# Optimization experiments

Hardware: AMD Instinct MI355X
Metric: run time of the kernel (lower is better)

## Reference

```python
import jax, jax.numpy as jnp
import numpy as np

DIM = 256
NUM_HEADS = 8
HEAD_DIM = DIM // NUM_HEADS
SCALE = HEAD_DIM ** -0.5


def setup_inputs() -> dict:
    key = jax.random.key(0)
    ks = jax.random.split(key, 12)
    B, NQ, S = 2, 1024, 8192
    inp = {
        "query_vectors": jax.random.normal(ks[0], (B, NQ, DIM), jnp.float32),
        "key_input_flatten": jax.random.normal(ks[1], (B, S, DIM), jnp.float32),
        "value_input_flatten": jax.random.normal(ks[2], (B, S, DIM), jnp.float32),
        "attention_mask": jax.random.randint(ks[3], (B, S), 0, 2).astype(jnp.float32),
        # Linear params (torch convention: y = x @ W.T + b)
        "Wq": jax.random.normal(ks[4], (DIM, DIM), jnp.float32) / np.sqrt(DIM),
        "bq": jnp.zeros((DIM,), jnp.float32),
        "Wk": jax.random.normal(ks[5], (DIM, DIM), jnp.float32) / np.sqrt(DIM),
        "bk": jnp.zeros((DIM,), jnp.float32),
        "Wv": jax.random.normal(ks[6], (DIM, DIM), jnp.float32) / np.sqrt(DIM),
        "bv": jnp.zeros((DIM,), jnp.float32),
        "Wo": jax.random.normal(ks[7], (DIM, DIM), jnp.float32) / np.sqrt(DIM),
        "bo": jnp.zeros((DIM,), jnp.float32),
    }
    return inp


def _split_heads(x):
    # (B, N, D) -> (B, H, N, hd)
    B, N, D = x.shape
    return x.reshape(B, N, NUM_HEADS, HEAD_DIM).transpose(0, 2, 1, 3)


def reference(query_vectors, key_input_flatten, value_input_flatten, attention_mask,
              Wq, bq, Wk, bk, Wv, bv, Wo, bo):
    B, NQ, D = query_vectors.shape
    q = _split_heads(query_vectors @ Wq.T + bq) * SCALE          # (B,H,NQ,hd)
    k = _split_heads(key_input_flatten @ Wk.T + bk)              # (B,H,S,hd)
    v = _split_heads(value_input_flatten @ Wv.T + bv)            # (B,H,S,hd)
    scores = jnp.einsum('bhqd,bhkd->bhqk', q, k)                 # (B,H,NQ,S)
    scores = scores + attention_mask[:, None, None, :] * -100.0
    finfo = jnp.finfo(scores.dtype)
    scores = jnp.clip(scores, finfo.min, finfo.max)
    probs = jax.nn.softmax(scores, axis=-1)
    ctx = jnp.einsum('bhqk,bhkd->bhqd', probs, v)                # (B,H,NQ,hd)
    ctx = ctx.transpose(0, 2, 1, 3).reshape(B, NQ, D)
    return ctx @ Wo.T + bo
```

## Files before the change

### kernel.cpp

```cpp
#include <hip/hip_runtime.h>
#include <hip/hip_bf16.h>

typedef __bf16 bf16x8 __attribute__((ext_vector_type(8)));
typedef __bf16 bf16x4 __attribute__((ext_vector_type(4)));
typedef float  f32x4  __attribute__((ext_vector_type(4)));

constexpr int BATCH = 2, H = 8, NQ = 1024, SEQ = 8192, DIM = 256, HD = 32;
constexpr int CHUNKS = 8, KVCHUNK = SEQ / CHUNKS;
constexpr float SCALE = 0.17677669529663687f;
constexpr float LOG2E = 1.4426950408889634f;
constexpr float QSCALE = SCALE * LOG2E;
constexpr float MASKC = 100.0f * LOG2E;
constexpr float MFIX  = 12.0f;

constexpr size_t OFF_QH   = 0;
constexpr size_t OFF_KH   = OFF_QH  + (size_t)BATCH*H*NQ*HD*2;
constexpr size_t OFF_VT   = OFF_KH  + (size_t)BATCH*H*SEQ*HD*2;
constexpr size_t OFF_CTX  = OFF_VT  + (size_t)BATCH*H*SEQ*HD*2;
constexpr size_t OFF_W    = OFF_CTX + (size_t)BATCH*NQ*DIM*4;
constexpr size_t OFF_PL   = OFF_W   + (size_t)4*DIM*DIM*2;
constexpr size_t OFF_BIAS = OFF_PL  + (size_t)CHUNKS*16*NQ*4;
constexpr size_t OFF_PO   = OFF_BIAS + (size_t)BATCH*SEQ*4;

__device__ __forceinline__ float fast_exp2(float x) {
    return __builtin_amdgcn_exp2f(x);
}

__global__ void prep_weights_kernel(const float* __restrict__ Wq, const float* __restrict__ Wk,
                                    const float* __restrict__ Wv, const float* __restrict__ Wo,
                                    const float* __restrict__ mask,
                                    __bf16* __restrict__ out, float* __restrict__ biasv) {
    int i = blockIdx.x * 256 + threadIdx.x;
    out[i]          = (__bf16)(Wq[i] * QSCALE);
    out[65536 + i]  = (__bf16)(Wk[i]);
    out[131072 + i] = (__bf16)(Wv[i]);
    out[196608 + i] = (__bf16)(Wo[i]);
    if (i < BATCH * SEQ)
        biasv[i] = -(mask[i] * MASKC + MFIX);
}

__global__ __launch_bounds__(256, 2)
void qkv_proj_kernel(const float* __restrict__ Xq, const float* __restrict__ Xk,
                     const float* __restrict__ Xv, const __bf16* __restrict__ Wb,
                     const float* __restrict__ bq, const float* __restrict__ bk,
                     const float* __restrict__ bv,
                     __bf16* __restrict__ qh, __bf16* __restrict__ kh, __bf16* __restrict__ vtp)
{
    __shared__ __bf16 Ash[128][72];
    __shared__ __bf16 Bsh[128][72];
    const int bid = blockIdx.x;
    const float* X; const __bf16* W; const float* bias; float bscale;
    __bf16* outp; int Mb, mode, lbid;
    if (bid < 32)       { X = Xq; W = Wb;          bias = bq; bscale = QSCALE; outp = qh;  Mb = NQ;  mode = 0; lbid = bid; }
    else if (bid < 288) { X = Xk; W = Wb + 65536;  bias = bk; bscale = 1.f;    outp = kh;  Mb = SEQ; mode = 0; lbid = bid - 32; }
    else                { X = Xv; W = Wb + 131072; bias = bv; bscale = 1.f;    outp = vtp; Mb = SEQ; mode = 1; lbid = bid - 288; }

    const int m0 = (lbid >> 1) * 128;
    const int n0 = (lbid & 1) * 128;
    const int t = threadIdx.x;
    const int w = t >> 6;
    const int lane = t & 63;
    const int g = lane >> 4;
    const int lr = lane & 15;
    const int wr = w >> 1, wc = w & 1;

    f32x4 acc[4][4] = {};

    for (int kk = 0; kk < DIM; kk += 64) {
        __syncthreads();
        #pragma unroll
        for (int i = 0; i < 8; ++i) {
            int c = i * 256 + t;
            int row = c >> 4;
            int q = c & 15;
            const float4 v = *reinterpret_cast<const float4*>(X + (size_t)(m0 + row) * DIM + kk + q * 4);
            bf16x4 bvv;
            bvv[0] = (__bf16)v.x; bvv[1] = (__bf16)v.y; bvv[2] = (__bf16)v.z; bvv[3] = (__bf16)v.w;
            *reinterpret_cast<bf16x4*>(&Ash[row][q * 4]) = bvv;
        }
        #pragma unroll
        for (int i = 0; i < 4; ++i) {
            int c = i * 256 + t;
            int row = c >> 3;
            int q = c & 7;
            *reinterpret_cast<bf16x8*>(&Bsh[row][q * 8]) =
                *reinterpret_cast<const bf16x8*>(W + (size_t)(n0 + row) * DIM + kk + q * 8);
        }
        __syncthreads();

        #pragma unroll
        for (int ks = 0; ks < 2; ++ks) {
            bf16x8 af[4], bfr[4];
            #pragma unroll
            for (int mt = 0; mt < 4; ++mt)
                af[mt] = *reinterpret_cast<const bf16x8*>(&Ash[wr * 64 + mt * 16 + lr][ks * 32 + g * 8]);
            #pragma unroll
            for (int nt = 0; nt < 4; ++nt)
                bfr[nt] = *reinterpret_cast<const bf16x8*>(&Bsh[wc * 64 + nt * 16 + lr][ks * 32 + g * 8]);
            if (mode == 1) {
                #pragma unroll
                for (int mt = 0; mt < 4; ++mt)
                    #pragma unroll
                    for (int nt = 0; nt < 4; ++nt)
                        acc[mt][nt] = __builtin_amdgcn_mfma_f32_16x16x32_bf16(bfr[nt], af[mt], acc[mt][nt], 0, 0, 0);
            } else {
                #pragma unroll
                for (int mt = 0; mt < 4; ++mt)
                    #pragma unroll
                    for (int nt = 0; nt < 4; ++nt)
                        acc[mt][nt] = __builtin_amdgcn_mfma_f32_16x16x32_bf16(af[mt], bfr[nt], acc[mt][nt], 0, 0, 0);
            }
        }
    }

    const int bb = m0 / Mb;
    const int sbase = m0 - bb * Mb + wr * 64;

    if (mode == 0) {
        #pragma unroll
        for (int nt = 0; nt < 4; ++nt) {
            int n = n0 + wc * 64 + nt * 16 + lr;
            float bvv = bias[n] * bscale;
            int h = n >> 5, hd = n & 31;
            __bf16* op = outp + ((size_t)(bb * H + h) * Mb) * 32 + hd;
            #pragma unroll
            for (int mt = 0; mt < 4; ++mt)
                #pragma unroll
                for (int r = 0; r < 4; ++r) {
                    int s = sbase + mt * 16 + g * 4 + r;
                    op[(size_t)s * 32] = (__bf16)(acc[mt][nt][r] + bvv);
                }
        }
    } else {
        #pragma unroll
        for (int nt = 0; nt < 4; ++nt)
            #pragma unroll
            for (int r = 0; r < 4; ++r) {
                int n = n0 + wc * 64 + nt * 16 + g * 4 + r;
                float bvv = bias[n] * bscale;
                int h = n >> 5, hd = n & 31;
                __bf16* op = outp + ((size_t)(bb * H + h) * 32 + hd) * SEQ;
                #pragma unroll
                for (int mt = 0; mt < 4; ++mt) {
                    int s = sbase + mt * 16 + lr;
                    op[s] = (__bf16)(acc[mt][nt][r] + bvv);
                }
            }
    }
}

__global__ __launch_bounds__(256, 2)
void oproj_kernel(const float* __restrict__ X, const __bf16* __restrict__ W,
                  const float* __restrict__ bias, float* __restrict__ outf)
{
    __shared__ __bf16 Ash[128][72];
    __shared__ __bf16 Bsh[128][72];
    const int m0 = (blockIdx.x >> 1) * 128;
    const int n0 = (blockIdx.x & 1) * 128;
    const int t = threadIdx.x;
    const int w = t >> 6;
    const int lane = t & 63;
    const int g = lane >> 4;
    const int lr = lane & 15;
    const int wr = w >> 1, wc = w & 1;

    f32x4 acc[4][4] = {};

    for (int kk = 0; kk < DIM; kk += 64) {
        __syncthreads();
        #pragma unroll
        for (int i = 0; i < 8; ++i) {
            int c = i * 256 + t;
            int row = c >> 4;
            int q = c & 15;
            const float4 v = *reinterpret_cast<const float4*>(X + (size_t)(m0 + row) * DIM + kk + q * 4);
            bf16x4 bvv;
            bvv[0] = (__bf16)v.x; bvv[1] = (__bf16)v.y; bvv[2] = (__bf16)v.z; bvv[3] = (__bf16)v.w;
            *reinterpret_cast<bf16x4*>(&Ash[row][q * 4]) = bvv;
        }
        #pragma unroll
        for (int i = 0; i < 4; ++i) {
            int c = i * 256 + t;
            int row = c >> 3;
            int q = c & 7;
            *reinterpret_cast<bf16x8*>(&Bsh[row][q * 8]) =
                *reinterpret_cast<const bf16x8*>(W + (size_t)(n0 + row) * DIM + kk + q * 8);
        }
        __syncthreads();

        #pragma unroll
        for (int ks = 0; ks < 2; ++ks) {
            bf16x8 af[4], bfr[4];
            #pragma unroll
            for (int mt = 0; mt < 4; ++mt)
                af[mt] = *reinterpret_cast<const bf16x8*>(&Ash[wr * 64 + mt * 16 + lr][ks * 32 + g * 8]);
            #pragma unroll
            for (int nt = 0; nt < 4; ++nt)
                bfr[nt] = *reinterpret_cast<const bf16x8*>(&Bsh[wc * 64 + nt * 16 + lr][ks * 32 + g * 8]);
            #pragma unroll
            for (int mt = 0; mt < 4; ++mt)
                #pragma unroll
                for (int nt = 0; nt < 4; ++nt)
                    acc[mt][nt] = __builtin_amdgcn_mfma_f32_16x16x32_bf16(af[mt], bfr[nt], acc[mt][nt], 0, 0, 0);
        }
    }

    #pragma unroll
    for (int nt = 0; nt < 4; ++nt) {
        int n = n0 + wc * 64 + nt * 16 + lr;
        float bvv = bias[n];
        #pragma unroll
        for (int mt = 0; mt < 4; ++mt)
            #pragma unroll
            for (int r = 0; r < 4; ++r) {
                int m = m0 + wr * 64 + mt * 16 + g * 4 + r;
                outf[(size_t)m * DIM + n] = acc[mt][nt][r] + bvv;
            }
    }
}

__global__ __launch_bounds__(256, 4)
void attn_kernel(const __bf16* __restrict__ qh, const __bf16* __restrict__ kh,
                 const __bf16* __restrict__ vt, const float* __restrict__ biasv,
                 float* __restrict__ Pl, float* __restrict__ Po)
{
    __shared__ __bf16 Ksh[64][40];
    __shared__ __bf16 Vsh[32][72];

    const int bid = blockIdx.x;
    const int bh = bid & 15;
    const int qt = (bid >> 4) & 7;
    const int ck = bid >> 7;
    const int b = bh >> 3;
    const int t = threadIdx.x;
    const int w = t >> 6, lane = t & 63, g = lane >> 4, lr = lane & 15;
    const int q0 = qt * 128 + w * 32;

    bf16x8 qf[2];
    #pragma unroll
    for (int qi = 0; qi < 2; ++qi)
        qf[qi] = *reinterpret_cast<const bf16x8*>(qh + ((size_t)bh * NQ + q0 + qi * 16 + lr) * HD + g * 8);

    const __bf16* kb = kh + (size_t)bh * SEQ * HD;
    const __bf16* vb = vt + (size_t)bh * HD * SEQ;
    const float* bvp = biasv + (size_t)b * SEQ;

    bf16x8 ones;
    #pragma unroll
    for (int i = 0; i < 8; ++i) ones[i] = (__bf16)1.0f;

    const int kr = t >> 2, kc = (t & 3) * 8;
    const int vr = t >> 3, vc = (t & 7) * 8;

    const int kv0 = ck * KVCHUNK;
    f32x4 o[2][2] = {};
    f32x4 l_acc[2] = {};

    for (int kv = kv0; kv < kv0 + KVCHUNK; kv += 64) {
        __syncthreads();
        *reinterpret_cast<bf16x8*>(&Ksh[kr][kc]) =
            *reinterpret_cast<const bf16x8*>(kb + (size_t)(kv + kr) * HD + kc);
        *reinterpret_cast<bf16x8*>(&Vsh[vr][vc]) =
            *reinterpret_cast<const bf16x8*>(vb + (size_t)vr * SEQ + kv + vc);
        __syncthreads();

        bf16x8 kf[4];
        #pragma unroll
        for (int j = 0; j < 4; ++j)
            kf[j] = *reinterpret_cast<const bf16x8*>(&Ksh[j * 16 + lr][g * 8]);

        bf16x4 vraw[2][4];
        #pragma unroll
        for (int hf = 0; hf < 2; ++hf)
            #pragma unroll
            for (int j = 0; j < 4; ++j)
                vraw[hf][j] = *reinterpret_cast<const bf16x4*>(&Vsh[hf * 16 + lr][j * 16 + g * 4]);
        bf16x8 vf[2][2];
        #pragma unroll
        for (int hf = 0; hf < 2; ++hf) {
            vf[hf][0] = __builtin_shufflevector(vraw[hf][0], vraw[hf][1], 0, 1, 2, 3, 4, 5, 6, 7);
            vf[hf][1] = __builtin_shufflevector(vraw[hf][2], vraw[hf][3], 0, 1, 2, 3, 4, 5, 6, 7);
        }

        f32x4 bc[4];
        #pragma unroll
        for (int j = 0; j < 4; ++j) {
            const float4 m4 = *reinterpret_cast<const float4*>(bvp + kv + j * 16 + g * 4);
            bc[j][0] = m4.x; bc[j][1] = m4.y; bc[j][2] = m4.z; bc[j][3] = m4.w;
        }

        #pragma unroll
        for (int qi = 0; qi < 2; ++qi) {
            f32x4 s[4];
            #pragma unroll
            for (int j = 0; j < 4; ++j)
                s[j] = __builtin_amdgcn_mfma_f32_16x16x32_bf16(kf[j], qf[qi], bc[j], 0, 0, 0);

            float p[16];
            #pragma unroll
            for (int j = 0; j < 4; ++j)
                #pragma unroll
                for (int r = 0; r < 4; ++r)
                    p[j * 4 + r] = fast_exp2(s[j][r]);

            bf16x8 pf0, pf1;
            #pragma unroll
            for (int i = 0; i < 8; ++i) { pf0[i] = (__bf16)p[i]; pf1[i] = (__bf16)p[8 + i]; }

            o[qi][0] = __builtin_amdgcn_mfma_f32_16x16x32_bf16(vf[0][0], pf0, o[qi][0], 0, 0, 0);
            o[qi][0] = __builtin_amdgcn_mfma_f32_16x16x32_bf16(vf[0][1], pf1, o[qi][0], 0, 0, 0);
            o[qi][1] = __builtin_amdgcn_mfma_f32_16x16x32_bf16(vf[1][0], pf0, o[qi][1], 0, 0, 0);
            o[qi][1] = __builtin_amdgcn_mfma_f32_16x16x32_bf16(vf[1][1], pf1, o[qi][1], 0, 0, 0);
            l_acc[qi] = __builtin_amdgcn_mfma_f32_16x16x32_bf16(ones, pf0, l_acc[qi], 0, 0, 0);
            l_acc[qi] = __builtin_amdgcn_mfma_f32_16x16x32_bf16(ones, pf1, l_acc[qi], 0, 0, 0);
        }
    }

    #pragma unroll
    for (int qi = 0; qi < 2; ++qi) {
        const int row = q0 + qi * 16 + lr;
        const size_t base = ((size_t)ck * 16 + bh) * NQ + row;
        if (g == 0) Pl[base] = l_acc[qi][0];
        #pragma unroll
        for (int hf = 0; hf < 2; ++hf)
            *reinterpret_cast<f32x4*>(Po + base * 32 + hf * 16 + g * 4) = o[qi][hf];
    }
}

__global__ __launch_bounds__(256)
void combine_kernel(const float* __restrict__ Pl, const float* __restrict__ Po,
                    float* __restrict__ ctx)
{
    const int idx = blockIdx.x * 256 + threadIdx.x;
    const int hd = idx & 31;
    const int row = (idx >> 5) & (NQ - 1);
    const int bh = idx >> 15;
    const int b = bh >> 3, h = bh & 7;

    float lsum = 0.f, osum = 0.f;
    #pragma unroll
    for (int c = 0; c < CHUNKS; ++c) {
        const size_t base = ((size_t)c * 16 + bh) * NQ + row;
        lsum += Pl[base];
        osum += Po[base * 32 + hd];
    }
    ctx[((size_t)b * NQ + row) * DIM + h * HD + hd] = osum / lsum;
}

extern "C" void kernel_launch(void* const* d_in, const int* in_sizes, int n_in,
                              void* d_out, int out_size, void* d_ws, size_t ws_size,
                              hipStream_t stream)
{
    const float* Xq   = (const float*)d_in[0];
    const float* Xk   = (const float*)d_in[1];
    const float* Xv   = (const float*)d_in[2];
    const float* mask = (const float*)d_in[3];
    const float* Wq   = (const float*)d_in[4];
    const float* bq   = (const float*)d_in[5];
    const float* Wk   = (const float*)d_in[6];
    const float* bk   = (const float*)d_in[7];
    const float* Wv   = (const float*)d_in[8];
    const float* bv   = (const float*)d_in[9];
    const float* Wo   = (const float*)d_in[10];
    const float* bo   = (const float*)d_in[11];

    char* ws = (char*)d_ws;
    __bf16* qh  = (__bf16*)(ws + OFF_QH);
    __bf16* kh  = (__bf16*)(ws + OFF_KH);
    __bf16* vtp = (__bf16*)(ws + OFF_VT);
    float*  ctx = (float*)(ws + OFF_CTX);
    __bf16* Wb  = (__bf16*)(ws + OFF_W);
    float*  Pl  = (float*)(ws + OFF_PL);
    float*  biasv = (float*)(ws + OFF_BIAS);
    float*  Po  = (float*)(ws + OFF_PO);

    prep_weights_kernel<<<256, 256, 0, stream>>>(Wq, Wk, Wv, Wo, mask, Wb, biasv);
    qkv_proj_kernel<<<544, 256, 0, stream>>>(Xq, Xk, Xv, Wb, bq, bk, bv, qh, kh, vtp);
    attn_kernel<<<16 * 8 * CHUNKS, 256, 0, stream>>>(qh, kh, vtp, biasv, Pl, Po);
    combine_kernel<<<16 * NQ * 32 / 256, 256, 0, stream>>>(Pl, Po, ctx);
    oproj_kernel<<<(BATCH * NQ / 128) * 2, 256, 0, stream>>>(ctx, Wb + 196608, bo, (float*)d_out);
}
```

Before: 73.60 us.

## Split attention block into 8 waves of 16 query rows each

Doubles the attention block to 512 threads, with each wave handling one 16-row query tile instead of two. Tile loads are redistributed to bf16x4 per thread. This aims for more resident waves to hide latency, at the cost of each wave re-reading the full K/V fragments from shared memory for half as many queries.

Result: slower. 80.41 us (+9.3%).

```diff
diff --git a/kernel.cpp b/kernel.cpp
--- a/kernel.cpp
+++ b/kernel.cpp
@@ -219,7 +219,7 @@
     }
 }
 
-__global__ __launch_bounds__(256, 4)
+__global__ __launch_bounds__(512)
 void attn_kernel(const __bf16* __restrict__ qh, const __bf16* __restrict__ kh,
                  const __bf16* __restrict__ vt, const float* __restrict__ biasv,
                  float* __restrict__ Pl, float* __restrict__ Po)
@@ -234,12 +234,9 @@
     const int b = bh >> 3;
     const int t = threadIdx.x;
     const int w = t >> 6, lane = t & 63, g = lane >> 4, lr = lane & 15;
-    const int q0 = qt * 128 + w * 32;
-
-    bf16x8 qf[2];
-    #pragma unroll
-    for (int qi = 0; qi < 2; ++qi)
-        qf[qi] = *reinterpret_cast<const bf16x8*>(qh + ((size_t)bh * NQ + q0 + qi * 16 + lr) * HD + g * 8);
+    const int q0 = qt * 128 + w * 16;
+
+    const bf16x8 qf = *reinterpret_cast<const bf16x8*>(qh + ((size_t)bh * NQ + q0 + lr) * HD + g * 8);
 
     const __bf16* kb = kh + (size_t)bh * SEQ * HD;
     const __bf16* vb = vt + (size_t)bh * HD * SEQ;
@@ -249,19 +246,19 @@
     #pragma unroll
     for (int i = 0; i < 8; ++i) ones[i] = (__bf16)1.0f;
 
-    const int kr = t >> 2, kc = (t & 3) * 8;
-    const int vr = t >> 3, vc = (t & 7) * 8;
+    const int kr = t >> 3, kc = (t & 7) * 4;
+    const int vr = t >> 4, vc = (t & 15) * 4;
 
     const int kv0 = ck * KVCHUNK;
-    f32x4 o[2][2] = {};
-    f32x4 l_acc[2] = {};
+    f32x4 o[2] = {};
+    f32x4 l_acc = {};
 
     for (int kv = kv0; kv < kv0 + KVCHUNK; kv += 64) {
         __syncthreads();
-        *reinterpret_cast<bf16x8*>(&Ksh[kr][kc]) =
-            *reinterpret_cast<const bf16x8*>(kb + (size_t)(kv + kr) * HD + kc);
-        *reinterpret_cast<bf16x8*>(&Vsh[vr][vc]) =
-            *reinterpret_cast<const bf16x8*>(vb + (size_t)vr * SEQ + kv + vc);
+        *reinterpret_cast<bf16x4*>(&Ksh[kr][kc]) =
+            *reinterpret_cast<const bf16x4*>(kb + (size_t)(kv + kr) * HD + kc);
+        *reinterpret_cast<bf16x4*>(&Vsh[vr][vc]) =
+            *reinterpret_cast<const bf16x4*>(vb + (size_t)vr * SEQ + kv + vc);
         __syncthreads();
 
         bf16x8 kf[4];
@@ -289,41 +286,37 @@
             bc[j][0] = m4.x; bc[j][1] = m4.y; bc[j][2] = m4.z; bc[j][3] = m4.w;
         }
 
-        #pragma unroll
-        for (int qi = 0; qi < 2; ++qi) {
-            f32x4 s[4];
-            #pragma unroll
-            for (int j = 0; j < 4; ++j)
-                s[j] = __builtin_amdgcn_mfma_f32_16x16x32_bf16(kf[j], qf[qi], bc[j], 0, 0, 0);
-
-            float p[16];
-            #pragma unroll
-            for (int j = 0; j < 4; ++j)
-                #pragma unroll
-                for (int r = 0; r < 4; ++r)
-                    p[j * 4 + r] = fast_exp2(s[j][r]);
-
-            bf16x8 pf0, pf1;
-            #pragma unroll
-            for (int i = 0; i < 8; ++i) { pf0[i] = (__bf16)p[i]; pf1[i] = (__bf16)p[8 + i]; }
-
-            o[qi][0] = __builtin_amdgcn_mfma_f32_16x16x32_bf16(vf[0][0], pf0, o[qi][0], 0, 0, 0);
-            o[qi][0] = __builtin_amdgcn_mfma_f32_16x16x32_bf16(vf[0][1], pf1, o[qi][0], 0, 0, 0);
-            o[qi][1] = __builtin_amdgcn_mfma_f32_16x16x32_bf16(vf[1][0], pf0, o[qi][1], 0, 0, 0);
-            o[qi][1] = __builtin_amdgcn_mfma_f32_16x16x32_bf16(vf[1][1], pf1, o[qi][1], 0, 0, 0);
-            l_acc[qi] = __builtin_amdgcn_mfma_f32_16x16x32_bf16(ones, pf0, l_acc[qi], 0, 0, 0);
-            l_acc[qi] = __builtin_amdgcn_mfma_f32_16x16x32_bf16(ones, pf1, l_acc[qi], 0, 0, 0);
-        }
-    }
-
-    #pragma unroll
-    for (int qi = 0; qi < 2; ++qi) {
-        const int row = q0 + qi * 16 + lr;
+        f32x4 s[4];
+        #pragma unroll
+        for (int j = 0; j < 4; ++j)
+            s[j] = __builtin_amdgcn_mfma_f32_16x16x32_bf16(kf[j], qf, bc[j], 0, 0, 0);
+
+        float p[16];
+        #pragma unroll
+        for (int j = 0; j < 4; ++j)
+            #pragma unroll
+            for (int r = 0; r < 4; ++r)
+                p[j * 4 + r] = fast_exp2(s[j][r]);
+
+        bf16x8 pf0, pf1;
+        #pragma unroll
+        for (int i = 0; i < 8; ++i) { pf0[i] = (__bf16)p[i]; pf1[i] = (__bf16)p[8 + i]; }
+
+        o[0] = __builtin_amdgcn_mfma_f32_16x16x32_bf16(vf[0][0], pf0, o[0], 0, 0, 0);
+        o[0] = __builtin_amdgcn_mfma_f32_16x16x32_bf16(vf[0][1], pf1, o[0], 0, 0, 0);
+        o[1] = __builtin_amdgcn_mfma_f32_16x16x32_bf16(vf[1][0], pf0, o[1], 0, 0, 0);
+        o[1] = __builtin_amdgcn_mfma_f32_16x16x32_bf16(vf[1][1], pf1, o[1], 0, 0, 0);
+        l_acc = __builtin_amdgcn_mfma_f32_16x16x32_bf16(ones, pf0, l_acc, 0, 0, 0);
+        l_acc = __builtin_amdgcn_mfma_f32_16x16x32_bf16(ones, pf1, l_acc, 0, 0, 0);
+    }
+
+    {
+        const int row = q0 + lr;
         const size_t base = ((size_t)ck * 16 + bh) * NQ + row;
-        if (g == 0) Pl[base] = l_acc[qi][0];
+        if (g == 0) Pl[base] = l_acc[0];
         #pragma unroll
         for (int hf = 0; hf < 2; ++hf)
-            *reinterpret_cast<f32x4*>(Po + base * 32 + hf * 16 + g * 4) = o[qi][hf];
+            *reinterpret_cast<f32x4*>(Po + base * 32 + hf * 16 + g * 4) = o[hf];
     }
 }
 
@@ -376,7 +369,7 @@
 
     prep_weights_kernel<<<256, 256, 0, stream>>>(Wq, Wk, Wv, Wo, mask, Wb, biasv);
     qkv_proj_kernel<<<544, 256, 0, stream>>>(Xq, Xk, Xv, Wb, bq, bk, bv, qh, kh, vtp);
-    attn_kernel<<<16 * 8 * CHUNKS, 256, 0, stream>>>(qh, kh, vtp, biasv, Pl, Po);
+    attn_kernel<<<16 * 8 * CHUNKS, 512, 0, stream>>>(qh, kh, vtp, biasv, Pl, Po);
     combine_kernel<<<16 * NQ * 32 / 256, 256, 0, stream>>>(Pl, Po, ctx);
     oproj_kernel<<<(BATCH * NQ / 128) * 2, 256, 0, stream>>>(ctx, Wb + 196608, bo, (float*)d_out);
 }
```
